# Optimization experiments

Hardware: AMD Instinct MI355X
Metric: run time of the kernel (lower is better)

The kernel has to match this reference:

```python
import jax, jax.numpy as jnp
import numpy as np

NUM_HEADS = 16
KEY_DIM = 64
NUM_FEATURES = 256
D_MODEL = NUM_HEADS * KEY_DIM
EPS = 1e-6


def softmax_kernel(data, proj):
    # data: [..., N, D], proj: [D, F]
    # Faithful to source: ratio uses proj.shape[0] (=D), matching the TF code.
    data_normalizer = 1.0 / jnp.sqrt(jnp.sqrt(jnp.asarray(data.shape[-1], data.dtype)))
    ratio = 1.0 / jnp.sqrt(jnp.asarray(proj.shape[0], data.dtype))
    data = data_normalizer * data
    data_dash = jnp.einsum('...nd,df->...nf', data, proj)
    diag = jnp.sum(jnp.square(data), axis=-1, keepdims=True)  # [..., N, 1]
    return ratio * (jnp.exp(data_dash - diag / 2.0) + EPS)


def setup_inputs() -> dict:
    key = jax.random.key(0)
    ks = jax.random.split(key, 12)
    B, N = 4, 4096
    s = 1.0 / np.sqrt(D_MODEL)
    inp = {
        'queries': jax.random.normal(ks[0], (B, N, D_MODEL), jnp.float32),
        'keys': jax.random.normal(ks[1], (B, N, D_MODEL), jnp.float32),
        'Wq': jax.random.normal(ks[2], (D_MODEL, D_MODEL), jnp.float32) * s,
        'bq': jnp.zeros((D_MODEL,), jnp.float32),
        'Wk': jax.random.normal(ks[3], (D_MODEL, D_MODEL), jnp.float32) * s,
        'bk': jnp.zeros((D_MODEL,), jnp.float32),
        'Wv': jax.random.normal(ks[4], (D_MODEL, D_MODEL), jnp.float32) * s,
        'bv': jnp.zeros((D_MODEL,), jnp.float32),
        'Wo': jax.random.normal(ks[5], (D_MODEL, D_MODEL), jnp.float32) * s,
        'bo': jnp.zeros((D_MODEL,), jnp.float32),
        # GlorotNormal for [KEY_DIM, NUM_FEATURES]
        'proj': jax.random.normal(ks[6], (KEY_DIM, NUM_FEATURES), jnp.float32)
                * np.sqrt(2.0 / (KEY_DIM + NUM_FEATURES)),
    }
    return inp


def reference(queries, keys, Wq, bq, Wk, bk, Wv, bv, Wo, bo, proj):
    # Original code uses x = queries for q, k, v (self-attention); keys arg unused.
    x = queries
    B, N, _ = x.shape
    H, D = NUM_HEADS, KEY_DIM

    def split_heads(t):
        return t.reshape(B, N, H, D).transpose(0, 2, 1, 3)  # [B,H,N,D]

    q = split_heads(x @ Wq + bq)
    k = split_heads(x @ Wk + bk)
    v = split_heads(x @ Wv + bv)

    q_prime = softmax_kernel(q, proj)  # [B,H,N,F]
    k_prime = softmax_kernel(k, proj)  # [B,H,N,F]

    kv = jnp.einsum('bhnf,bhnd->bhfd', k_prime, v)        # [B,H,F,D]
    qkv = jnp.einsum('bhnf,bhfd->bhnd', q_prime, kv)       # [B,H,N,D]
    k_sum = jnp.sum(k_prime, axis=2)                        # [B,H,F]
    norm = jnp.einsum('bhnf,bhf->bhn', q_prime, k_sum) + EPS
    qkv = qkv / norm[..., None]

    out = qkv.transpose(0, 2, 1, 3).reshape(B, N, H * D)    # [B,N,d_model]
    return out @ Wo + bo
```

## Files before the change

### kernel.cpp

```cpp
#include <hip/hip_runtime.h>

typedef __attribute__((ext_vector_type(8))) short short8;
typedef __attribute__((ext_vector_type(4))) float f32x4;

#define MFMA16 __builtin_amdgcn_mfma_f32_16x16x32_bf16

#define GLOAD16(gp, lp) __builtin_amdgcn_global_load_lds(                      \
    (const __attribute__((address_space(1))) void*)(gp),                       \
    (__attribute__((address_space(3))) void*)(lp), 16, 0, 0)

__device__ __forceinline__ unsigned short f2bf(float f) {
  unsigned int u = __float_as_uint(f);
  unsigned int r = u + 0x7fffu + ((u >> 16) & 1u);
  return (unsigned short)(r >> 16);
}
__device__ __forceinline__ float bf2f(unsigned short h) {
  return __uint_as_float(((unsigned int)h) << 16);
}

__global__ __launch_bounds__(256) void cast_x_kernel(
    const float* __restrict__ in, unsigned short* __restrict__ out, int n4) {
  int i = blockIdx.x * 256 + threadIdx.x;
  if (i >= n4) return;
  float4 v = reinterpret_cast<const float4*>(in)[i];
  ushort4 o;
  o.x = f2bf(v.x); o.y = f2bf(v.y); o.z = f2bf(v.z); o.w = f2bf(v.w);
  reinterpret_cast<ushort4*>(out)[i] = o;
}

__global__ __launch_bounds__(256) void tcast_f32_kernel(
    const float* __restrict__ in, unsigned short* __restrict__ out, int R, int C) {
  __shared__ float t[64][65];
  int c0 = blockIdx.x * 64, r0 = blockIdx.y * 64;
  int tx = threadIdx.x, ty = threadIdx.y;
#pragma unroll
  for (int i = 0; i < 16; ++i)
    t[ty + 4 * i][tx] = in[(size_t)(r0 + ty + 4 * i) * C + c0 + tx];
  __syncthreads();
#pragma unroll
  for (int i = 0; i < 16; ++i)
    out[(size_t)(c0 + ty + 4 * i) * R + r0 + tx] = f2bf(t[tx][ty + 4 * i]);
}

__global__ __launch_bounds__(256) void tcast4_kernel(
    const float* __restrict__ i0, const float* __restrict__ i1,
    const float* __restrict__ i2, const float* __restrict__ i3,
    unsigned short* __restrict__ o0, unsigned short* __restrict__ o1,
    unsigned short* __restrict__ o2, unsigned short* __restrict__ o3) {
  const float* in = i0; unsigned short* out = o0;
  if (blockIdx.z == 1) { in = i1; out = o1; }
  else if (blockIdx.z == 2) { in = i2; out = o2; }
  else if (blockIdx.z == 3) { in = i3; out = o3; }
  __shared__ float t[64][65];
  int c0 = blockIdx.x * 64, r0 = blockIdx.y * 64;
  int tx = threadIdx.x, ty = threadIdx.y;
#pragma unroll
  for (int i = 0; i < 16; ++i)
    t[ty + 4 * i][tx] = in[(size_t)(r0 + ty + 4 * i) * 1024 + c0 + tx];
  __syncthreads();
#pragma unroll
  for (int i = 0; i < 16; ++i)
    out[(size_t)(c0 + ty + 4 * i) * 1024 + r0 + tx] = f2bf(t[tx][ty + 4 * i]);
}

template <int OUTF>
__global__ __launch_bounds__(256) void gemm_bt_kernel(
    const unsigned short* __restrict__ A,
    const unsigned short* W0, const unsigned short* W1, const unsigned short* W2,
    const float* b0, const float* b1, const float* b2,
    void* o0, void* o1, void* o2) {
  constexpr int KD = 1024, ND = 1024;
  int m0, n0, z;
  if constexpr (OUTF == 3) {
    int id = blockIdx.x;
    int g = id / 24, slot = id - g * 24;
    z = slot >> 3;
    int t = g * 8 + (slot & 7);
    m0 = (t & 127) * 128;
    n0 = (t >> 7) * 128;
  } else {
    m0 = blockIdx.x * 128;
    n0 = blockIdx.y * 128;
    z = 0;
  }
  const unsigned short* W = W0; const float* bias = b0; void* op = o0;
  if (z == 1) { W = W1; bias = b1; op = o1; }
  else if (z == 2) { W = W2; bias = b2; op = o2; }

  __shared__ unsigned short lsA[128 * 32];
  __shared__ unsigned short lsB[128 * 32];
  extern __shared__ unsigned short tt[];
  int tid = threadIdx.x;
  int w = tid >> 6, lane = tid & 63;
  int lo = lane & 15, hi = lane >> 4;
  int wm = (w >> 1) * 64, wn = (w & 1) * 64;

  int srow0 = (w * 2 + 0) * 16 + (lane >> 2);
  int srow1 = (w * 2 + 1) * 16 + (lane >> 2);
  int scol = (lane & 3) * 8;
  const unsigned short* gA0 = A + (size_t)(m0 + srow0) * KD + scol;
  const unsigned short* gA1 = A + (size_t)(m0 + srow1) * KD + scol;
  const unsigned short* gB0 = W + (size_t)(n0 + srow0) * KD + scol;
  const unsigned short* gB1 = W + (size_t)(n0 + srow1) * KD + scol;
  unsigned short* lA0 = &lsA[(w * 2 + 0) * 512];
  unsigned short* lA1 = &lsA[(w * 2 + 1) * 512];
  unsigned short* lB0 = &lsB[(w * 2 + 0) * 512];
  unsigned short* lB1 = &lsB[(w * 2 + 1) * 512];

  f32x4 acc[4][4];
#pragma unroll
  for (int fm = 0; fm < 4; ++fm)
#pragma unroll
    for (int fn = 0; fn < 4; ++fn) acc[fm][fn] = (f32x4){0.f, 0.f, 0.f, 0.f};

  for (int kt = 0; kt < KD; kt += 32) {
    GLOAD16(gA0 + kt, lA0);
    GLOAD16(gA1 + kt, lA1);
    GLOAD16(gB0 + kt, lB0);
    GLOAD16(gB1 + kt, lB1);
    __syncthreads();
    short8 af[4], bfr[4];
#pragma unroll
    for (int fm = 0; fm < 4; ++fm)
      af[fm] = *reinterpret_cast<const short8*>(
          &lsA[(wm + fm * 16 + lo) * 32 + hi * 8]);
#pragma unroll
    for (int fn = 0; fn < 4; ++fn)
      bfr[fn] = *reinterpret_cast<const short8*>(
          &lsB[(wn + fn * 16 + lo) * 32 + hi * 8]);
#pragma unroll
    for (int fm = 0; fm < 4; ++fm)
#pragma unroll
      for (int fn = 0; fn < 4; ++fn)
        acc[fm][fn] = MFMA16(af[fm], bfr[fn], acc[fm][fn], 0, 0, 0);
    __syncthreads();
  }

  bool vpath = (OUTF == 3) && (z == 2);
#pragma unroll
  for (int fn = 0; fn < 4; ++fn) {
    int coll = wn + fn * 16 + lo;
    float bv = bias[n0 + coll];
#pragma unroll
    for (int fm = 0; fm < 4; ++fm) {
#pragma unroll
      for (int j = 0; j < 4; ++j) {
        int rowl = wm + fm * 16 + hi * 4 + j;
        float v = acc[fm][fn][j] + bv;
        if constexpr (OUTF == 1) {
          reinterpret_cast<float*>(op)[(size_t)(m0 + rowl) * ND + n0 + coll] = v;
        } else {
          if (vpath)
            tt[coll * 136 + rowl] = f2bf(v);
          else
            reinterpret_cast<unsigned short*>(op)[(size_t)(m0 + rowl) * ND + n0 + coll] =
                f2bf(v);
        }
      }
    }
  }
  if constexpr (OUTF == 3) {
    if (vpath) {
      __syncthreads();
      int b = m0 >> 12, tok0 = m0 & 4095;
      int c = tid >> 1, half = (tid & 1) * 64;
      unsigned short* dst = reinterpret_cast<unsigned short*>(op) +
                            (size_t)(b * 1024 + n0 + c) * 4096 + tok0 + half;
#pragma unroll
      for (int i = 0; i < 8; ++i) {
        short8 vv = *reinterpret_cast<const short8*>(&tt[c * 136 + half + i * 8]);
        *reinterpret_cast<short8*>(dst + i * 8) = vv;
      }
    }
  }
}

__global__ __launch_bounds__(256) void kv_fused_kernel(
    const unsigned short* __restrict__ K, const unsigned short* __restrict__ PT,
    const unsigned short* __restrict__ VT,
    float* __restrict__ kvp, float* __restrict__ ksp) {
  __shared__ unsigned short kp[256 * 40];
  int s = blockIdx.x, bh = blockIdx.y, b = bh >> 4, h = bh & 15;
  int tid = threadIdx.x, w = tid >> 6, lane = tid & 63;
  int lo = lane & 15, hi = lane >> 4;
  int f0w = w * 64;

  short8 pb[4][2];
#pragma unroll
  for (int fn = 0; fn < 4; ++fn) {
    int f = f0w + fn * 16 + lo;
    pb[fn][0] = *reinterpret_cast<const short8*>(PT + (size_t)f * 64 + hi * 8);
    pb[fn][1] = *reinterpret_cast<const short8*>(PT + (size_t)f * 64 + 32 + hi * 8);
  }
  const unsigned short* vbase[4];
#pragma unroll
  for (int fn = 0; fn < 4; ++fn)
    vbase[fn] = VT + (size_t)(bh * 64 + fn * 16 + lo) * 4096;

  f32x4 acck[4][4];
#pragma unroll
  for (int fm = 0; fm < 4; ++fm)
#pragma unroll
    for (int fn = 0; fn < 4; ++fn) acck[fm][fn] = (f32x4){0.f, 0.f, 0.f, 0.f};
  float ks[4] = {0.f, 0.f, 0.f, 0.f};

  for (int c = 0; c < 16; ++c) {
    int n0 = s * 512 + c * 32;
    const unsigned short* Ab = K + (size_t)(b * 4096 + n0) * 1024 + h * 64;
    short8 af[2][2], b2[4];
#pragma unroll
    for (int fm = 0; fm < 2; ++fm)
#pragma unroll
      for (int kt = 0; kt < 2; ++kt)
        af[fm][kt] = *reinterpret_cast<const short8*>(
            Ab + (size_t)(fm * 16 + lo) * 1024 + kt * 32 + hi * 8);
#pragma unroll
    for (int fn = 0; fn < 4; ++fn)
      b2[fn] = *reinterpret_cast<const short8*>(vbase[fn] + n0 + hi * 8);

    float dp[2] = {0.f, 0.f};
#pragma unroll
    for (int fm = 0; fm < 2; ++fm)
#pragma unroll
      for (int kt = 0; kt < 2; ++kt)
#pragma unroll
        for (int j = 0; j < 8; ++j) {
          float qv = bf2f((unsigned short)af[fm][kt][j]);
          dp[fm] += qv * qv;
        }
#pragma unroll
    for (int fm = 0; fm < 2; ++fm) {
      dp[fm] += __shfl_xor(dp[fm], 16);
      dp[fm] += __shfl_xor(dp[fm], 32);
    }
    f32x4 accf[2][4];
#pragma unroll
    for (int fm = 0; fm < 2; ++fm)
#pragma unroll
      for (int fn = 0; fn < 4; ++fn) accf[fm][fn] = (f32x4){0.f, 0.f, 0.f, 0.f};
#pragma unroll
    for (int fn = 0; fn < 4; ++fn) {
      accf[0][fn] = MFMA16(af[0][0], pb[fn][0], accf[0][fn], 0, 0, 0);
      accf[0][fn] = MFMA16(af[0][1], pb[fn][1], accf[0][fn], 0, 0, 0);
      accf[1][fn] = MFMA16(af[1][0], pb[fn][0], accf[1][fn], 0, 0, 0);
      accf[1][fn] = MFMA16(af[1][1], pb[fn][1], accf[1][fn], 0, 0, 0);
    }
#pragma unroll
    for (int fm = 0; fm < 2; ++fm)
#pragma unroll
      for (int fn = 0; fn < 4; ++fn) {
        ushort4 pk;
#pragma unroll
        for (int j = 0; j < 4; ++j) {
          float dg = __shfl(dp[fm], hi * 4 + j);
          float v = 0.125f *
                    (__expf(0.35355339059327373f * accf[fm][fn][j] - 0.0625f * dg) + 1e-6f);
          ks[fn] += v;
          ((unsigned short*)&pk)[j] = f2bf(v);
        }
        *reinterpret_cast<ushort4*>(&kp[(f0w + fn * 16 + lo) * 40 + fm * 16 + hi * 4]) = pk;
      }
    short8 a2[4];
#pragma unroll
    for (int fm = 0; fm < 4; ++fm)
      a2[fm] = *reinterpret_cast<const short8*>(&kp[(f0w + fm * 16 + lo) * 40 + hi * 8]);
#pragma unroll
    for (int fm = 0; fm < 4; ++fm)
#pragma unroll
      for (int fn = 0; fn < 4; ++fn)
        acck[fm][fn] = MFMA16(a2[fm], b2[fn], acck[fm][fn], 0, 0, 0);
  }
#pragma unroll
  for (int fn = 0; fn < 4; ++fn) {
    float v = ks[fn];
    v += __shfl_xor(v, 16);
    v += __shfl_xor(v, 32);
    if (hi == 0)
      ksp[(size_t)(s * 64 + bh) * 256 + f0w + fn * 16 + lo] = v;
  }
#pragma unroll
  for (int fm = 0; fm < 4; ++fm)
#pragma unroll
    for (int fn = 0; fn < 4; ++fn)
#pragma unroll
      for (int j = 0; j < 4; ++j)
        kvp[((size_t)(s * 64 + bh) * 256 + f0w + fm * 16 + hi * 4 + j) * 64 + fn * 16 + lo] =
            acck[fm][fn][j];
}

__global__ __launch_bounds__(256) void kvred_kernel(
    const float* __restrict__ kvp, const float* __restrict__ ksp,
    unsigned short* __restrict__ kvT, float* __restrict__ ksum) {
  __shared__ float t[64][65];
  int bh = blockIdx.x, g = blockIdx.y, tid = threadIdx.x;
  int fbase = g * 64;
  int fo = tid >> 2, dq = (tid & 3) * 16;
  float sum[16];
#pragma unroll
  for (int i = 0; i < 16; ++i) sum[i] = 0.f;
#pragma unroll
  for (int s = 0; s < 8; ++s) {
    const float* base = kvp + ((size_t)(s * 64 + bh) * 256 + fbase + fo) * 64 + dq;
#pragma unroll
    for (int i = 0; i < 16; ++i) sum[i] += base[i];
  }
#pragma unroll
  for (int i = 0; i < 16; ++i) t[fo][dq + i] = sum[i];
  __syncthreads();
  int d = tid >> 2, fq = (tid & 3) * 16;
  unsigned short wv[16];
#pragma unroll
  for (int i = 0; i < 16; ++i) wv[i] = f2bf(t[fq + i][d]);
  unsigned short* dst = kvT + (size_t)(bh * 64 + d) * 256 + fbase + fq;
  *reinterpret_cast<short8*>(dst) = *reinterpret_cast<const short8*>(&wv[0]);
  *reinterpret_cast<short8*>(dst + 8) = *reinterpret_cast<const short8*>(&wv[8]);
  if (g == 0) {
    float tsum = 0.f;
#pragma unroll
    for (int s = 0; s < 8; ++s) tsum += ksp[(size_t)(s * 64 + bh) * 256 + tid];
    ksum[bh * 256 + tid] = tsum;
  }
}

__global__ __launch_bounds__(256) void qkv_fused_kernel(
    const unsigned short* __restrict__ Q, const unsigned short* __restrict__ PT,
    const unsigned short* __restrict__ KVT, const float* __restrict__ KSUM,
    unsigned short* __restrict__ Y) {
  __shared__ unsigned short qp[128 * 128];
  int bh = blockIdx.y, b = bh >> 4, h = bh & 15;
  int t0 = blockIdx.x * 128;
  int tid = threadIdx.x, w = tid >> 6, lane = tid & 63;
  int lo = lane & 15, hi = lane >> 4;
  int r0 = w * 32;
  const unsigned short* Ab = Q + (size_t)(b * 4096 + t0 + r0) * 1024 + h * 64;

  float ksr[16];
#pragma unroll
  for (int fn = 0; fn < 16; ++fn) ksr[fn] = KSUM[bh * 256 + fn * 16 + lo];

  short8 af[2][2];
  float dp[2] = {0.f, 0.f};
#pragma unroll
  for (int fm = 0; fm < 2; ++fm)
#pragma unroll
    for (int kt = 0; kt < 2; ++kt) {
      af[fm][kt] = *reinterpret_cast<const short8*>(
          Ab + (size_t)(fm * 16 + lo) * 1024 + kt * 32 + hi * 8);
#pragma unroll
      for (int j = 0; j < 8; ++j) {
        float qv = bf2f((unsigned short)af[fm][kt][j]);
        dp[fm] += qv * qv;
      }
    }
#pragma unroll
  for (int fm = 0; fm < 2; ++fm) {
    dp[fm] += __shfl_xor(dp[fm], 16);
    dp[fm] += __shfl_xor(dp[fm], 32);
  }

  float np[2][4] = {{0.f, 0.f, 0.f, 0.f}, {0.f, 0.f, 0.f, 0.f}};
  f32x4 acco[2][4];
#pragma unroll
  for (int fm = 0; fm < 2; ++fm)
#pragma unroll
    for (int fn = 0; fn < 4; ++fn) acco[fm][fn] = (f32x4){0.f, 0.f, 0.f, 0.f};

#pragma unroll
  for (int hf = 0; hf < 2; ++hf) {
    f32x4 accf[2][8];
#pragma unroll
    for (int fm = 0; fm < 2; ++fm)
#pragma unroll
      for (int fn = 0; fn < 8; ++fn) accf[fm][fn] = (f32x4){0.f, 0.f, 0.f, 0.f};
#pragma unroll
    for (int fn = 0; fn < 8; ++fn) {
      int f = hf * 128 + fn * 16 + lo;
      short8 pb0 = *reinterpret_cast<const short8*>(PT + (size_t)f * 64 + hi * 8);
      short8 pb1 = *reinterpret_cast<const short8*>(PT + (size_t)f * 64 + 32 + hi * 8);
      accf[0][fn] = MFMA16(af[0][0], pb0, accf[0][fn], 0, 0, 0);
      accf[0][fn] = MFMA16(af[0][1], pb1, accf[0][fn], 0, 0, 0);
      accf[1][fn] = MFMA16(af[1][0], pb0, accf[1][fn], 0, 0, 0);
      accf[1][fn] = MFMA16(af[1][1], pb1, accf[1][fn], 0, 0, 0);
    }
#pragma unroll
    for (int fm = 0; fm < 2; ++fm)
#pragma unroll
      for (int fn = 0; fn < 8; ++fn)
#pragma unroll
        for (int j = 0; j < 4; ++j) {
          float dg = __shfl(dp[fm], hi * 4 + j);
          float v = 0.125f *
                    (__expf(0.35355339059327373f * accf[fm][fn][j] - 0.0625f * dg) + 1e-6f);
          np[fm][j] += v * ksr[hf * 8 + fn];
          int row = r0 + fm * 16 + hi * 4 + j;
          int fl = fn * 16 + lo;
          int byt = (row * 256 + fl * 2) ^ ((row & 7) << 4);
          *reinterpret_cast<unsigned short*>(reinterpret_cast<char*>(qp) + byt) = f2bf(v);
        }
#pragma unroll
    for (int kt2 = 0; kt2 < 4; ++kt2) {
      short8 a2[2], b2[4];
#pragma unroll
      for (int fm = 0; fm < 2; ++fm) {
        int row = r0 + fm * 16 + lo;
        int byt = (row * 256 + kt2 * 64 + hi * 16) ^ ((row & 7) << 4);
        a2[fm] = *reinterpret_cast<const short8*>(reinterpret_cast<char*>(qp) + byt);
      }
#pragma unroll
      for (int fn = 0; fn < 4; ++fn)
        b2[fn] = *reinterpret_cast<const short8*>(
            KVT + (size_t)(bh * 64 + fn * 16 + lo) * 256 + hf * 128 + kt2 * 32 + hi * 8);
#pragma unroll
      for (int fm = 0; fm < 2; ++fm)
#pragma unroll
        for (int fn = 0; fn < 4; ++fn)
          acco[fm][fn] = MFMA16(a2[fm], b2[fn], acco[fm][fn], 0, 0, 0);
    }
  }
#pragma unroll
  for (int fm = 0; fm < 2; ++fm)
#pragma unroll
    for (int j = 0; j < 4; ++j) {
      np[fm][j] += __shfl_xor(np[fm][j], 1);
      np[fm][j] += __shfl_xor(np[fm][j], 2);
      np[fm][j] += __shfl_xor(np[fm][j], 4);
      np[fm][j] += __shfl_xor(np[fm][j], 8);
    }
#pragma unroll
  for (int fm = 0; fm < 2; ++fm)
#pragma unroll
    for (int j = 0; j < 4; ++j) {
      float nv = np[fm][j] + 1e-6f;
      int row = b * 4096 + t0 + r0 + fm * 16 + hi * 4 + j;
#pragma unroll
      for (int fn = 0; fn < 4; ++fn)
        Y[(size_t)row * 1024 + h * 64 + fn * 16 + lo] = f2bf(acco[fm][fn][j] / nv);
    }
}

extern "C" void kernel_launch(void* const* d_in, const int* in_sizes, int n_in,
                              void* d_out, int out_size, void* d_ws, size_t ws_size,
                              hipStream_t stream) {
  (void)in_sizes; (void)n_in; (void)out_size; (void)ws_size;
  const float* x    = (const float*)d_in[0];
  const float* Wq   = (const float*)d_in[2];
  const float* bq   = (const float*)d_in[3];
  const float* Wk   = (const float*)d_in[4];
  const float* bk   = (const float*)d_in[5];
  const float* Wv   = (const float*)d_in[6];
  const float* bv   = (const float*)d_in[7];
  const float* Wo   = (const float*)d_in[8];
  const float* bo   = (const float*)d_in[9];
  const float* proj = (const float*)d_in[10];
  float* out = (float*)d_out;

  constexpr size_t SZ_XB = (size_t)16384 * 1024 * 2;
  constexpr size_t SZ_W  = (size_t)1024 * 1024 * 2;
  constexpr size_t SZ_PT = (size_t)256 * 64 * 2;

  char* p = (char*)d_ws;
  size_t off = 0;
  char* a_xb  = p + off; off += SZ_XB;
  char* a_WqT = p + off; off += SZ_W;
  char* a_WkT = p + off; off += SZ_W;
  char* a_WvT = p + off; off += SZ_W;
  char* a_WoT = p + off; off += SZ_W;
  char* a_pT  = p + off; off += SZ_PT;
  char* a_qb  = p + off; off += SZ_XB;
  char* a_kb  = p + off; off += SZ_XB;
  char* a_ksp  = p + off; off += (size_t)8 * 64 * 256 * 4;
  char* a_kvT  = p + off; off += (size_t)64 * 64 * 256 * 2;
  char* a_ksum = p + off; off += (size_t)64 * 256 * 4;

  char* a_kvp = a_xb;
  char* a_vT = (char*)d_out;
  char* a_y = a_kb;

  dim3 tb(64, 4);

  cast_x_kernel<<<16384, 256, 0, stream>>>(x, (unsigned short*)a_xb, 16384 * 1024 / 4);
  tcast4_kernel<<<dim3(16, 16, 4), tb, 0, stream>>>(
      Wq, Wk, Wv, Wo,
      (unsigned short*)a_WqT, (unsigned short*)a_WkT,
      (unsigned short*)a_WvT, (unsigned short*)a_WoT);
  tcast_f32_kernel<<<dim3(4, 1), tb, 0, stream>>>(proj, (unsigned short*)a_pT, 64, 256);

  gemm_bt_kernel<3><<<3072, 256, 128 * 136 * 2, stream>>>(
      (unsigned short*)a_xb,
      (unsigned short*)a_WqT, (unsigned short*)a_WkT, (unsigned short*)a_WvT,
      bq, bk, bv, a_qb, a_kb, a_vT);

  kv_fused_kernel<<<dim3(8, 64), 256, 0, stream>>>(
      (unsigned short*)a_kb, (unsigned short*)a_pT, (unsigned short*)a_vT,
      (float*)a_kvp, (float*)a_ksp);
  kvred_kernel<<<dim3(64, 4), 256, 0, stream>>>(
      (float*)a_kvp, (float*)a_ksp, (unsigned short*)a_kvT, (float*)a_ksum);

  qkv_fused_kernel<<<dim3(32, 64), 256, 0, stream>>>(
      (unsigned short*)a_qb, (unsigned short*)a_pT, (unsigned short*)a_kvT,
      (float*)a_ksum, (unsigned short*)a_y);

  gemm_bt_kernel<1><<<dim3(128, 8, 1), 256, 0, stream>>>(
      (unsigned short*)a_y,
      (unsigned short*)a_WoT, nullptr, nullptr,
      bo, nullptr, nullptr, out, nullptr, nullptr);
}
```

Baseline: 341.5 us.

## Double-buffer A tiles in LDS, load B fragments directly from global

The GEMM main loop now double-buffers only the A tile in LDS, prefetching the next k-slice while computing on the current one. The B (weight) fragments are read straight from global memory into registers, which removes the B LDS staging. The V-transpose epilogue reuses the A buffer in four 32-column passes, so no dynamic shared memory is needed. LDS use drops from roughly 50KB to 16KB, which should allow more resident blocks. The cost is uncoalesced, uncached-in-LDS global loads for B that are re-read by each wave, and extra barriers in the epilogue.

```diff
diff --git a/kernel.cpp b/kernel.cpp
--- a/kernel.cpp
+++ b/kernel.cpp
@@ -87,9 +87,7 @@
   if (z == 1) { W = W1; bias = b1; op = o1; }
   else if (z == 2) { W = W2; bias = b2; op = o2; }
 
-  __shared__ unsigned short lsA[128 * 32];
-  __shared__ unsigned short lsB[128 * 32];
-  extern __shared__ unsigned short tt[];
+  __shared__ unsigned short lsA[2][4096];
   int tid = threadIdx.x;
   int w = tid >> 6, lane = tid & 63;
   int lo = lane & 15, hi = lane >> 4;
@@ -100,12 +98,11 @@
   int scol = (lane & 3) * 8;
   const unsigned short* gA0 = A + (size_t)(m0 + srow0) * KD + scol;
   const unsigned short* gA1 = A + (size_t)(m0 + srow1) * KD + scol;
-  const unsigned short* gB0 = W + (size_t)(n0 + srow0) * KD + scol;
-  const unsigned short* gB1 = W + (size_t)(n0 + srow1) * KD + scol;
-  unsigned short* lA0 = &lsA[(w * 2 + 0) * 512];
-  unsigned short* lA1 = &lsA[(w * 2 + 1) * 512];
-  unsigned short* lB0 = &lsB[(w * 2 + 0) * 512];
-  unsigned short* lB1 = &lsB[(w * 2 + 1) * 512];
+
+  const unsigned short* gBf[4];
+#pragma unroll
+  for (int fn = 0; fn < 4; ++fn)
+    gBf[fn] = W + (size_t)(n0 + wn + fn * 16 + lo) * KD + hi * 8;
 
   f32x4 acc[4][4];
 #pragma unroll
@@ -113,64 +110,85 @@
 #pragma unroll
     for (int fn = 0; fn < 4; ++fn) acc[fm][fn] = (f32x4){0.f, 0.f, 0.f, 0.f};
 
+  GLOAD16(gA0, &lsA[0][(w * 2 + 0) * 512]);
+  GLOAD16(gA1, &lsA[0][(w * 2 + 1) * 512]);
+  __syncthreads();
+
+#pragma unroll 2
   for (int kt = 0; kt < KD; kt += 32) {
-    GLOAD16(gA0 + kt, lA0);
-    GLOAD16(gA1 + kt, lA1);
-    GLOAD16(gB0 + kt, lB0);
-    GLOAD16(gB1 + kt, lB1);
-    __syncthreads();
-    short8 af[4], bfr[4];
+    int buf = (kt >> 5) & 1;
+    short8 bfr[4];
+#pragma unroll
+    for (int fn = 0; fn < 4; ++fn)
+      bfr[fn] = *reinterpret_cast<const short8*>(gBf[fn] + kt);
+    __builtin_amdgcn_sched_barrier(0);
+    if (kt + 32 < KD) {
+      GLOAD16(gA0 + kt + 32, &lsA[buf ^ 1][(w * 2 + 0) * 512]);
+      GLOAD16(gA1 + kt + 32, &lsA[buf ^ 1][(w * 2 + 1) * 512]);
+    }
+    __builtin_amdgcn_sched_barrier(0);
+    short8 af[4];
 #pragma unroll
     for (int fm = 0; fm < 4; ++fm)
       af[fm] = *reinterpret_cast<const short8*>(
-          &lsA[(wm + fm * 16 + lo) * 32 + hi * 8]);
-#pragma unroll
-    for (int fn = 0; fn < 4; ++fn)
-      bfr[fn] = *reinterpret_cast<const short8*>(
-          &lsB[(wn + fn * 16 + lo) * 32 + hi * 8]);
+          &lsA[buf][(wm + fm * 16 + lo) * 32 + hi * 8]);
 #pragma unroll
     for (int fm = 0; fm < 4; ++fm)
 #pragma unroll
       for (int fn = 0; fn < 4; ++fn)
         acc[fm][fn] = MFMA16(af[fm], bfr[fn], acc[fm][fn], 0, 0, 0);
+    __builtin_amdgcn_sched_barrier(0);
     __syncthreads();
   }
 
   bool vpath = (OUTF == 3) && (z == 2);
-#pragma unroll
-  for (int fn = 0; fn < 4; ++fn) {
-    int coll = wn + fn * 16 + lo;
-    float bv = bias[n0 + coll];
-#pragma unroll
-    for (int fm = 0; fm < 4; ++fm) {
-#pragma unroll
-      for (int j = 0; j < 4; ++j) {
-        int rowl = wm + fm * 16 + hi * 4 + j;
-        float v = acc[fm][fn][j] + bv;
-        if constexpr (OUTF == 1) {
-          reinterpret_cast<float*>(op)[(size_t)(m0 + rowl) * ND + n0 + coll] = v;
-        } else {
-          if (vpath)
-            tt[coll * 136 + rowl] = f2bf(v);
+  if (!vpath) {
+#pragma unroll
+    for (int fn = 0; fn < 4; ++fn) {
+      int coll = wn + fn * 16 + lo;
+      float bv = bias[n0 + coll];
+#pragma unroll
+      for (int fm = 0; fm < 4; ++fm) {
+#pragma unroll
+        for (int j = 0; j < 4; ++j) {
+          int rowl = wm + fm * 16 + hi * 4 + j;
+          float v = acc[fm][fn][j] + bv;
+          if constexpr (OUTF == 1)
+            reinterpret_cast<float*>(op)[(size_t)(m0 + rowl) * ND + n0 + coll] = v;
           else
             reinterpret_cast<unsigned short*>(op)[(size_t)(m0 + rowl) * ND + n0 + coll] =
                 f2bf(v);
         }
       }
     }
-  }
-  if constexpr (OUTF == 3) {
-    if (vpath) {
+  } else {
+    unsigned short* tt = &lsA[0][0];
+    int b = m0 >> 12, tok0 = m0 & 4095;
+    int c2 = tid >> 3, q = (tid & 7) * 16;
+#pragma unroll
+    for (int p = 0; p < 4; ++p) {
       __syncthreads();
-      int b = m0 >> 12, tok0 = m0 & 4095;
-      int c = tid >> 1, half = (tid & 1) * 64;
+      if (wn == (p >> 1) * 64) {
+        int fb = (p & 1) * 2;
+#pragma unroll
+        for (int fi = 0; fi < 2; ++fi) {
+          int fn = fb + fi;
+          int cp = fi * 16 + lo;
+          float bv = bias[n0 + p * 32 + cp];
+#pragma unroll
+          for (int fm = 0; fm < 4; ++fm)
+#pragma unroll
+            for (int j = 0; j < 4; ++j)
+              tt[cp * 136 + wm + fm * 16 + hi * 4 + j] = f2bf(acc[fm][fn][j] + bv);
+        }
+      }
+      __syncthreads();
       unsigned short* dst = reinterpret_cast<unsigned short*>(op) +
-                            (size_t)(b * 1024 + n0 + c) * 4096 + tok0 + half;
-#pragma unroll
-      for (int i = 0; i < 8; ++i) {
-        short8 vv = *reinterpret_cast<const short8*>(&tt[c * 136 + half + i * 8]);
-        *reinterpret_cast<short8*>(dst + i * 8) = vv;
-      }
+                            (size_t)(b * 1024 + n0 + p * 32 + c2) * 4096 + tok0 + q;
+      *reinterpret_cast<short8*>(dst) =
+          *reinterpret_cast<const short8*>(&tt[c2 * 136 + q]);
+      *reinterpret_cast<short8*>(dst + 8) =
+          *reinterpret_cast<const short8*>(&tt[c2 * 136 + q + 8]);
     }
   }
 }
@@ -485,7 +503,7 @@
       (unsigned short*)a_WvT, (unsigned short*)a_WoT);
   tcast_f32_kernel<<<dim3(4, 1), tb, 0, stream>>>(proj, (unsigned short*)a_pT, 64, 256);
 
-  gemm_bt_kernel<3><<<3072, 256, 128 * 136 * 2, stream>>>(
+  gemm_bt_kernel<3><<<3072, 256, 0, stream>>>(
       (unsigned short*)a_xb,
       (unsigned short*)a_WqT, (unsigned short*)a_WkT, (unsigned short*)a_WvT,
       bq, bk, bv, a_qb, a_kb, a_vT);
```

Result: slower. 469.5 us (+37.5%).
